# Kernel optimization log

Measured on AMD Instinct MI355X. Metric: run time of the kernel, lower is better.

The kernel has to match this reference:

```python
import jax, jax.numpy as jnp
import numpy as np


def _jacobian_circulant(v):
    """Spatial Jacobian of a 3D vector field with circulant boundaries.

    v : (B, X, Y, Z, D) velocity field (channels last)
    returns J : (B, X, Y, Z, D, D) with J[..., i, j] = d v_i / d x_j,
    computed by central differences with wrap-around (circulant) bounds.
    """
    cols = []
    for j in range(3):
        ax = 1 + j  # spatial axis for coordinate j
        g = (jnp.roll(v, -1, axis=ax) - jnp.roll(v, 1, axis=ax)) * 0.5
        cols.append(g)
    return jnp.stack(cols, axis=-1)  # (B, X, Y, Z, D, D)


def _bracket(x, y):
    """Lie bracket of two velocity fields: [x, y] = J_x y - J_y x."""
    jx = _jacobian_circulant(x)
    jy = _jacobian_circulant(y)
    return (jnp.einsum('bxyzij,bxyzj->bxyzi', jx, y)
            - jnp.einsum('bxyzij,bxyzj->bxyzi', jy, x))


def _bch(x, y, trunc=2):
    """Truncated BCH series: z s.t. exp(z) = exp(x) o exp(y)."""
    z = x + y
    if trunc >= 2:
        z = z + 0.5 * _bracket(x, y)
    return z


def setup_inputs() -> dict:
    key = jax.random.key(0)
    k1, k2 = jax.random.split(key)
    B, D, X, Y, Z = 2, 3, 128, 128, 128
    left = jax.random.normal(k1, (B, D, X, Y, Z), dtype=jnp.float32)
    right = jax.random.normal(k2, (B, D, X, Y, Z), dtype=jnp.float32)
    return {"left": left, "right": right}


def reference(left, right):
    # (B, D, *shape) -> channels-last (B, *shape, D)
    l = jnp.moveaxis(left, 1, -1)
    r = jnp.moveaxis(right, 1, -1)
    v = _bch(l, r, trunc=2)
    return jnp.moveaxis(v, -1, 1)
```

## Files before the change

### kernel.cpp

```cpp
#include <hip/hip_runtime.h>


namespace {
constexpr int Xd = 128, Yd = 128, Zd = 128, Dd = 3;
constexpr int Sd  = Xd * Yd * Zd;
constexpr int YZd = Yd * Zd;
constexpr int XSEG = 8;
constexpr int YT   = 8;
constexpr int ZC   = 32;

__device__ inline float4 f4sub(float4 a, float4 b) {
    return make_float4(a.x - b.x, a.y - b.y, a.z - b.z, a.w - b.w);
}
__device__ inline float4 f4add(float4 a, float4 b) {
    return make_float4(a.x + b.x, a.y + b.y, a.z + b.z, a.w + b.w);
}
__device__ inline float4 f4mul(float4 a, float4 b) {
    return make_float4(a.x * b.x, a.y * b.y, a.z * b.z, a.w * b.w);
}
__device__ inline float4 f4fma(float4 a, float4 b, float4 c) {
    return make_float4(fmaf(a.x, b.x, c.x), fmaf(a.y, b.y, c.y),
                       fmaf(a.z, b.z, c.z), fmaf(a.w, b.w, c.w));
}
__device__ inline float4 f4fms(float4 a, float4 b, float4 c) {
    return make_float4(fmaf(-a.x, b.x, c.x), fmaf(-a.y, b.y, c.y),
                       fmaf(-a.z, b.z, c.z), fmaf(-a.w, b.w, c.w));
}
}

__global__ void __launch_bounds__(256, 2)
bch_march(const float* __restrict__ L, const float* __restrict__ R,
          float* __restrict__ O)
{
    __shared__ float4 sP[2 * Dd][YT][ZC];

    const int t  = threadIdx.x;
    const int zc = t & 31;
    const int ly = t >> 5;

    int bb = blockIdx.x;
    const int xs = bb & 15; bb >>= 4;
    const int yt = bb & 15; bb >>= 4;
    const int b  = bb;

    const int y  = yt * YT + ly;
    const int z0 = zc * 4;
    const int x0 = xs * XSEG;

    const int fbase = b * (Dd * Sd) + y * Zd + z0;
    const float* pL = L + fbase;
    const float* pR = R + fbase;
    float*       pO = O + fbase;

    const int oym = (((y - 1) & 127) - y) * Zd;
    const int oyp = (((y + 1) & 127) - y) * Zd;
    const int zlm = (zc + 31) & 31;
    const int zlp = (zc + 1) & 31;

    float4 AL[3], AR[3], BL[3], BR[3], CL[3], CR[3], DL[3], DR[3];

    auto loadP = [&](float4 (&PL)[3], float4 (&PR)[3], int xp) {
        const int off = xp * YZd;
#pragma unroll
        for (int d = 0; d < 3; ++d) {
            PL[d] = *(const float4*)(pL + off + d * Sd);
            PR[d] = *(const float4*)(pR + off + d * Sd);
        }
    };

    loadP(AL, AR, (x0 + 127) & 127);
    loadP(BL, BR, x0);
    loadP(CL, CR, (x0 + 1) & 127);

#pragma unroll
    for (int s = 0; s < XSEG; ++s) {
        const int x    = x0 + s;
        const int xoff = x * YZd;

        if (s < XSEG - 1) loadP(DL, DR, (x + 2) & 127);

        float4 HmL[3], HmR[3], HpL[3], HpR[3];
        if (ly == 0) {
#pragma unroll
            for (int d = 0; d < 3; ++d) {
                HmL[d] = *(const float4*)(pL + xoff + oym + d * Sd);
                HmR[d] = *(const float4*)(pR + xoff + oym + d * Sd);
            }
        }
        if (ly == YT - 1) {
#pragma unroll
            for (int d = 0; d < 3; ++d) {
                HpL[d] = *(const float4*)(pL + xoff + oyp + d * Sd);
                HpR[d] = *(const float4*)(pR + xoff + oyp + d * Sd);
            }
        }

#pragma unroll
        for (int d = 0; d < 3; ++d) {
            sP[d][ly][zc]     = BL[d];
            sP[3 + d][ly][zc] = BR[d];
        }
        __syncthreads();

        const int lym = (ly == 0) ? 0 : ly - 1;
        const int lyp = (ly == YT - 1) ? YT - 1 : ly + 1;
        float4 yLm[3], yRm[3], yLp[3], yRp[3];
#pragma unroll
        for (int d = 0; d < 3; ++d) {
            yLm[d] = sP[d][lym][zc];     if (ly == 0)      yLm[d] = HmL[d];
            yRm[d] = sP[3 + d][lym][zc]; if (ly == 0)      yRm[d] = HmR[d];
            yLp[d] = sP[d][lyp][zc];     if (ly == YT - 1) yLp[d] = HpL[d];
            yRp[d] = sP[3 + d][lyp][zc]; if (ly == YT - 1) yRp[d] = HpR[d];
        }

#pragma unroll
        for (int i = 0; i < 3; ++i) {
            float4 dl = f4sub(CL[i], AL[i]);
            float4 dr = f4sub(CR[i], AR[i]);
            float4 br = f4fms(dr, BL[0], f4mul(dl, BR[0]));

            dl = f4sub(yLp[i], yLm[i]);
            dr = f4sub(yRp[i], yRm[i]);
            br = f4fms(dr, BL[1], f4fma(dl, BR[1], br));

            const float lzm = __shfl(BL[i].w, zlm, 32);
            const float lzp = __shfl(BL[i].x, zlp, 32);
            const float rzm = __shfl(BR[i].w, zlm, 32);
            const float rzp = __shfl(BR[i].x, zlp, 32);
            dl = make_float4(BL[i].y - lzm, BL[i].z - BL[i].x,
                             BL[i].w - BL[i].y, lzp - BL[i].z);
            dr = make_float4(BR[i].y - rzm, BR[i].z - BR[i].x,
                             BR[i].w - BR[i].y, rzp - BR[i].z);
            br = f4fms(dr, BL[2], f4fma(dl, BR[2], br));

            float4 out = f4add(BL[i], BR[i]);
            const float4 q = make_float4(0.25f, 0.25f, 0.25f, 0.25f);
            out = f4fma(q, br, out);
            *(float4*)(pO + xoff + i * Sd) = out;
        }
        __syncthreads();

        if (s < XSEG - 1) {
#pragma unroll
            for (int d = 0; d < 3; ++d) {
                AL[d] = BL[d]; BL[d] = CL[d]; CL[d] = DL[d];
                AR[d] = BR[d]; BR[d] = CR[d]; CR[d] = DR[d];
            }
        }
    }
}

extern "C" void kernel_launch(void* const* d_in, const int* in_sizes, int n_in,
                              void* d_out, int out_size, void* d_ws, size_t ws_size,
                              hipStream_t stream)
{
    const float* L = (const float*)d_in[0];
    const float* R = (const float*)d_in[1];
    float*       O = (float*)d_out;

    const int nblocks = 2 * (Yd / YT) * (Xd / XSEG);
    bch_march<<<dim3(nblocks), dim3(256), 0, stream>>>(L, R, O);
}
```

Before: 141.7 us.

## Halve x-march length, stage y-halo rows in shared memory, use nontemporal stores

Cuts the per-block x segment from 8 to 4 planes, doubling the block count, and raises the launch-bounds occupancy hint from 2 to 4 blocks per CU. The y-halo rows are now written into two extra padded rows of the shared tile, so every thread reads its y neighbours from LDS without per-thread select branches. Output stores use nontemporal hints to avoid polluting cache. The shorter march re-reads more x-halo planes, and the tighter register cap may cause spills.

```diff
diff --git a/kernel.cpp b/kernel.cpp
--- a/kernel.cpp
+++ b/kernel.cpp
@@ -5,9 +5,11 @@
 constexpr int Xd = 128, Yd = 128, Zd = 128, Dd = 3;
 constexpr int Sd  = Xd * Yd * Zd;
 constexpr int YZd = Yd * Zd;
-constexpr int XSEG = 8;
+constexpr int XSEG = 4;
 constexpr int YT   = 8;
 constexpr int ZC   = 32;
+
+typedef float f32x4_t __attribute__((ext_vector_type(4)));
 
 __device__ inline float4 f4sub(float4 a, float4 b) {
     return make_float4(a.x - b.x, a.y - b.y, a.z - b.z, a.w - b.w);
@@ -26,20 +28,23 @@
     return make_float4(fmaf(-a.x, b.x, c.x), fmaf(-a.y, b.y, c.y),
                        fmaf(-a.z, b.z, c.z), fmaf(-a.w, b.w, c.w));
 }
+__device__ inline void store_nt(float* p, float4 v) {
+    __builtin_nontemporal_store(*(const f32x4_t*)&v, (f32x4_t*)p);
+}
 }
 
-__global__ void __launch_bounds__(256, 2)
+__global__ void __launch_bounds__(256, 4)
 bch_march(const float* __restrict__ L, const float* __restrict__ R,
           float* __restrict__ O)
 {
-    __shared__ float4 sP[2 * Dd][YT][ZC];
+    __shared__ float4 sP[2 * Dd][YT + 2][ZC];
 
     const int t  = threadIdx.x;
     const int zc = t & 31;
     const int ly = t >> 5;
 
     int bb = blockIdx.x;
-    const int xs = bb & 15; bb >>= 4;
+    const int xs = bb & 31; bb >>= 5;
     const int yt = bb & 15; bb >>= 4;
     const int b  = bb;
 
@@ -72,45 +77,44 @@
     loadP(BL, BR, x0);
     loadP(CL, CR, (x0 + 1) & 127);
 
+    const bool lo = (ly == 0);
+    const bool hi = (ly == YT - 1);
+    const int  oyh = lo ? oym : oyp;
+    const int  hrow = lo ? 0 : YT + 1;
+
 #pragma unroll
     for (int s = 0; s < XSEG; ++s) {
-        const int x    = x0 + s;
-        const int xoff = x * YZd;
+        const int xoff = (x0 + s) * YZd;
 
-        if (s < XSEG - 1) loadP(DL, DR, (x + 2) & 127);
+        if (s < XSEG - 1) loadP(DL, DR, (x0 + s + 2) & 127);
 
-        float4 HmL[3], HmR[3], HpL[3], HpR[3];
-        if (ly == 0) {
+        float4 H[6];
+        if (lo | hi) {
 #pragma unroll
             for (int d = 0; d < 3; ++d) {
-                HmL[d] = *(const float4*)(pL + xoff + oym + d * Sd);
-                HmR[d] = *(const float4*)(pR + xoff + oym + d * Sd);
-            }
-        }
-        if (ly == YT - 1) {
-#pragma unroll
-            for (int d = 0; d < 3; ++d) {
-                HpL[d] = *(const float4*)(pL + xoff + oyp + d * Sd);
-                HpR[d] = *(const float4*)(pR + xoff + oyp + d * Sd);
+                H[d]     = *(const float4*)(pL + xoff + oyh + d * Sd);
+                H[3 + d] = *(const float4*)(pR + xoff + oyh + d * Sd);
             }
         }
 
 #pragma unroll
         for (int d = 0; d < 3; ++d) {
-            sP[d][ly][zc]     = BL[d];
-            sP[3 + d][ly][zc] = BR[d];
+            sP[d][ly + 1][zc]     = BL[d];
+            sP[3 + d][ly + 1][zc] = BR[d];
+        }
+        if (lo | hi) {
+#pragma unroll
+            for (int d = 0; d < 6; ++d) sP[d][hrow][zc] = H[d];
         }
         __syncthreads();
 
-        const int lym = (ly == 0) ? 0 : ly - 1;
-        const int lyp = (ly == YT - 1) ? YT - 1 : ly + 1;
         float4 yLm[3], yRm[3], yLp[3], yRp[3];
 #pragma unroll
         for (int d = 0; d < 3; ++d) {
-            yLm[d] = sP[d][lym][zc];     if (ly == 0)      yLm[d] = HmL[d];
-            yRm[d] = sP[3 + d][lym][zc]; if (ly == 0)      yRm[d] = HmR[d];
-            yLp[d] = sP[d][lyp][zc];     if (ly == YT - 1) yLp[d] = HpL[d];
-            yRp[d] = sP[3 + d][lyp][zc]; if (ly == YT - 1) yRp[d] = HpR[d];
+            yLm[d] = sP[d][ly][zc];
+            yLp[d] = sP[d][ly + 2][zc];
+            yRm[d] = sP[3 + d][ly][zc];
+            yRp[d] = sP[3 + d][ly + 2][zc];
         }
 
 #pragma unroll
@@ -136,7 +140,7 @@
             float4 out = f4add(BL[i], BR[i]);
             const float4 q = make_float4(0.25f, 0.25f, 0.25f, 0.25f);
             out = f4fma(q, br, out);
-            *(float4*)(pO + xoff + i * Sd) = out;
+            store_nt(pO + xoff + i * Sd, out);
         }
         __syncthreads();
 
```

Measured after the change: 196.9 us. 1.39x slower.
